# Kernel tuning notes

Hardware: AMD Instinct MI355X
Metric: run time of the kernel (lower is better)

The kernel has to match this reference:

```python
import jax, jax.numpy as jnp
import numpy as np

B, H, W = 8, 1080, 1920


def setup_inputs() -> dict:
    key = jax.random.key(0)
    k1, k2 = jax.random.split(key)
    flow = jax.random.normal(k1, (B, 2, H, W), jnp.float32) * 10.0  # ~10px motion
    depth = jax.random.uniform(k2, (B, 1, H, W), jnp.float32) + 0.1  # positive weight
    return {"flow": flow, "depth": depth}


def _splat_avg(flow, depth):
    """Depth-weighted forward splat of -flow to the 4 integer pixels around the
    projected location (x+fx, y+fy), accumulate a weight buffer, then average."""
    Bn, _, Hn, Wn = flow.shape
    fx, fy = flow[:, 0], flow[:, 1]                 # [B,H,W]
    col = jnp.arange(Wn, dtype=flow.dtype)
    row = jnp.arange(Hn, dtype=flow.dtype)[:, None]
    x2 = col + fx
    y2 = row + fy
    valid = (x2 >= 0) & (x2 <= Wn - 1) & (y2 >= 0) & (y2 <= Hn - 1)
    ixL = jnp.clip(jnp.floor(x2).astype(jnp.int32), 0, Wn - 1)
    iyT = jnp.clip(jnp.floor(y2).astype(jnp.int32), 0, Hn - 1)
    ixR = jnp.minimum(ixL + 1, Wn - 1)
    iyB = jnp.minimum(iyT + 1, Hn - 1)
    w = jnp.where(valid, depth[:, 0], 0.0)          # depth weight, 0 if off-frame
    b_off = (jnp.arange(Bn, dtype=jnp.int32) * (Hn * Wn))[:, None, None]
    corners = [(iyT, ixL), (iyT, ixR), (iyB, ixL), (iyB, ixR)]
    lin = jnp.stack([b_off + iy * Wn + ix for iy, ix in corners]).reshape(-1)  # [4*B*H*W]
    vals = jnp.stack([-fx * w, -fy * w, w])         # [3,B,H,W]
    vals = jnp.broadcast_to(vals[:, None], (3, 4, Bn, Hn, Wn)).reshape(3, -1)
    acc = jnp.zeros((3, Bn * Hn * Wn), flow.dtype).at[:, lin].add(vals)
    out = acc[:2].reshape(2, Bn, Hn, Wn).transpose(1, 0, 2, 3)   # [B,2,H,W]
    count = acc[2].reshape(Bn, 1, Hn, Wn)                        # [B,1,H,W]
    denom = jnp.where(count > 0, count, 1.0)
    out = out / denom                                            # avg pass
    return out, count


def _fillhole(out, count):
    """For hole pixels (count==0), average the nearest filled pixel found in
    each of the 4 axis directions (left/right/up/down), equal weights."""
    mask = count[:, 0] > 0                           # [B,H,W]
    Bn, Hn, Wn = mask.shape
    col = jnp.arange(Wn, dtype=jnp.int32)
    row = jnp.arange(Hn, dtype=jnp.int32)[:, None]

    a = jnp.where(mask, col, -1)
    incl = jax.lax.associative_scan(jnp.maximum, a, axis=2)
    left = jnp.pad(incl[:, :, :-1], ((0, 0), (0, 0), (1, 0)), constant_values=-1)
    a = jnp.where(mask, col, Wn)
    incl = jax.lax.associative_scan(jnp.minimum, a, axis=2, reverse=True)
    right = jnp.pad(incl[:, :, 1:], ((0, 0), (0, 0), (0, 1)), constant_values=Wn)
    a = jnp.where(mask, row, -1)
    incl = jax.lax.associative_scan(jnp.maximum, a, axis=1)
    up = jnp.pad(incl[:, :-1, :], ((0, 0), (1, 0), (0, 0)), constant_values=-1)
    a = jnp.where(mask, row, Hn)
    incl = jax.lax.associative_scan(jnp.minimum, a, axis=1, reverse=True)
    down = jnp.pad(incl[:, 1:, :], ((0, 0), (0, 1), (0, 0)), constant_values=Hn)

    def gather(idx, axis, bound):
        found = ((idx >= 0) & (idx < bound))[:, None]        # [B,1,H,W]
        ic = jnp.clip(idx, 0, bound - 1)[:, None]
        v = jnp.take_along_axis(out, jnp.broadcast_to(ic, out.shape), axis=axis)
        return v, found.astype(out.dtype)

    vl, wl = gather(left, 3, Wn)
    vr, wr = gather(right, 3, Wn)
    vu, wu = gather(up, 2, Hn)
    vd, wd = gather(down, 2, Hn)
    s = wl + wr + wu + wd
    fill = (wl * vl + wr * vr + wu * vu + wd * vd) / jnp.maximum(s, 1.0)
    hole = (~mask)[:, None]
    return jnp.where(hole & (s > 0), fill, out)


def reference(flow, depth):
    out, count = _splat_avg(flow, depth)
    out = _fillhole(out, count)   # torch module runs fillhole when requires_grad=False
    return out
```

## Files before the change

### kernel.cpp

```cpp
#include <hip/hip_runtime.h>

#define BB 8
#define HH 1080
#define WW 1920
constexpr int HWc  = HH * WW;
constexpr int Ntot = BB * HWc;

constexpr int TILE = 64;
constexpr int MAR  = 32;
constexpr int REG  = TILE + 2 * MAR;
constexpr int WT   = WW / TILE;
constexpr int HT   = (HH + TILE - 1) / TILE;
constexpr int NTILE = WT * HT;
constexpr int GT    = NTILE * BB;
constexpr int CAP   = 256;

constexpr int SDIM = 65;
constexpr int SSTR = 66;
constexpr int PL   = SSTR * SSTR;

static_assert(TILE == 64, "ownership test uses >>6");
static_assert((WW & 3) == 0 && (HWc & 3) == 0, "float4 groups must not straddle");
static_assert(3 * PL * 4 <= 53000, "need 3 blocks/CU");

constexpr size_t OFF_BKT  = 16384;
constexpr size_t OFF_MASK = OFF_BKT + (size_t)GT * CAP * 16;
constexpr size_t OFF_W    = OFF_MASK + (size_t)Ntot;
static_assert(OFF_W % 16 == 0, "wplane must be float4-aligned");

__device__ inline void spill_append(int b, int xs, int ys, int ixL, int iyT,
                                    float fx, float fy, float w,
                                    unsigned* cnt, float4* buckets) {
    int ixR = min(ixL + 1, WW - 1);
    int iyB = min(iyT + 1, HH - 1);
    int cxs[2] = {ixL, ixR};
    int cys[2] = {iyT, iyB};
    float vx = -fx * w, vy = -fy * w;
#pragma unroll
    for (int a = 0; a < 2; ++a)
#pragma unroll
        for (int cc = 0; cc < 2; ++cc) {
            int cx = cxs[cc], cy = cys[a];
            int ox = (cx >> 6) * TILE - MAR;
            int oy = (cy >> 6) * TILE - MAR;
            if (!(xs >= ox && xs < ox + REG && ys >= oy && ys < oy + REG)) {
                int gtile = b * NTILE + (cy >> 6) * WT + (cx >> 6);
                unsigned slot = atomicAdd(&cnt[gtile], 1u);
                if (slot < (unsigned)CAP) {
                    float4 rec;
                    rec.x = __int_as_float(((cy & 63) << 6) | (cx & 63));
                    rec.y = vx; rec.z = vy; rec.w = w;
                    buckets[(size_t)gtile * CAP + slot] = rec;
                }
            }
        }
}

#define PROC(FXC, FYC, DWC, CGX)                                               \
    {                                                                          \
        float fx = (FXC), fy = (FYC);                                          \
        float x2 = (float)(CGX) + fx, y2 = gyf + fy;                           \
        if (x2 >= 0.f && x2 <= (float)(WW - 1) &&                              \
            y2 >= 0.f && y2 <= (float)(HH - 1)) {                              \
            int ixL = (int)floorf(x2);        \
            int iyT = (int)floorf(y2);                                         \
            unsigned cI = (unsigned)(ixL - (X0 - 1));                          \
            unsigned rI = (unsigned)(iyT - (Y0 - 1));                          \
            if (cI < (unsigned)SDIM && rI < (unsigned)SDIM) {                  \
                float w = (DWC);                                               \
                if (ixL == WW - 1) w += w;      \
                if (iyT == HH - 1) w += w;      \
                int cell = (int)(rI * SSTR + cI);                              \
                atomicAdd(&sm[cell],          -fx * w);                        \
                atomicAdd(&sm[cell + PL],     -fy * w);                        \
                atomicAdd(&sm[cell + 2 * PL], w);                              \
            }                                                                  \
            if (core && (fabsf(fx) > 30.f || fabsf(fy) > 30.f))                \
                spill_append(b, (CGX), gy, ixL, iyT, fx, fy, (DWC),            \
                             cnt, buckets);                                    \
        }                                                                      \
    }

__global__ __launch_bounds__(512, 6) void tile_k(const float* __restrict__ flow,
                                                 const float* __restrict__ depth,
                                                 unsigned* __restrict__ cnt,
                                                 float4* __restrict__ buckets,
                                                 float* __restrict__ out,
                                                 unsigned char* __restrict__ mask,
                                                 float* __restrict__ wplane) {
    __shared__ float sm[3 * PL];
    const int bid  = blockIdx.x;
    const int b    = bid & 7;
    const int tile = bid >> 3;
    const int ty   = tile / WT;
    const int tx   = tile - ty * WT;
    const int X0 = tx * TILE, Y0 = ty * TILE;
    const int rx0 = X0 - MAR, ry0 = Y0 - MAR;
    const int tid = threadIdx.x;

    float4* sm4 = (float4*)sm;
    for (int i = tid; i < 3 * PL / 4; i += 512)
        sm4[i] = make_float4(0.f, 0.f, 0.f, 0.f);
    __syncthreads();

    const float* fxp = flow + (size_t)b * 2 * HWc;
    const float* fyp = fxp + HWc;
    const float* dp  = depth + (size_t)b * HWc;

    const int gx  = rx0 + ((tid & 31) << 2);
    const bool xok = (unsigned)gx < (unsigned)WW;
    const bool xin = (unsigned)(gx - X0) < (unsigned)TILE;
    int gy = ry0 + (tid >> 5);
    float4 cfx, cfy, cd;
    bool ok = xok && ((unsigned)gy < (unsigned)HH);
    if (ok) {
        int p = gy * WW + gx;
        cfx = *(const float4*)(fxp + p);
        cfy = *(const float4*)(fyp + p);
        cd  = *(const float4*)(dp + p);
    }
#pragma unroll
    for (int k = 0; k < 8; ++k) {
        float4 nfx, nfy, nd;
        bool nok = false;
        const int ngy = gy + 16;
        if (k < 7) {
            nok = xok && ((unsigned)ngy < (unsigned)HH);
            if (nok) {
                int np = ngy * WW + gx;
                nfx = *(const float4*)(fxp + np);
                nfy = *(const float4*)(fyp + np);
                nd  = *(const float4*)(dp + np);
            }
        }
        if (ok) {
            const float gyf = (float)gy;
            const bool core = xin && ((unsigned)(gy - Y0) < (unsigned)TILE);
            PROC(cfx.x, cfy.x, cd.x, gx)
            PROC(cfx.y, cfy.y, cd.y, gx + 1)
            PROC(cfx.z, cfy.z, cd.z, gx + 2)
            PROC(cfx.w, cfy.w, cd.w, gx + 3)
        }
        ok = nok; gy = ngy; cfx = nfx; cfy = nfy; cd = nd;
    }
    __syncthreads();

    float* o0 = out + (size_t)b * 2 * HWc;
    float* o1 = o0 + HWc;
    float* wp = wplane + (size_t)b * HWc;
    unsigned char* mb = mask + (size_t)b * HWc;
#pragma unroll
    for (int k = 0; k < 2; ++k) {
        int j   = k * 512 + tid;
        int row = j >> 4;
        int gy2 = Y0 + row;
        if (gy2 < HH) {
            int c0 = (j & 15) << 2;
            int q  = gy2 * WW + X0 + c0;
            const int rA = (row + 1) * SSTR + c0;
            const int rB = row * SSTR + c0;
            float4 vx, vy, wv;
            {
                float a_0 = sm[rA], a_1 = sm[rA+1], a_2 = sm[rA+2], a_3 = sm[rA+3], a_4 = sm[rA+4];
                float b_0 = sm[rB], b_1 = sm[rB+1], b_2 = sm[rB+2], b_3 = sm[rB+3], b_4 = sm[rB+4];
                vx.x = a_0+a_1+b_0+b_1; vx.y = a_1+a_2+b_1+b_2;
                vx.z = a_2+a_3+b_2+b_3; vx.w = a_3+a_4+b_3+b_4;
            }
            {
                const int oA = rA + PL, oB = rB + PL;
                float a_0 = sm[oA], a_1 = sm[oA+1], a_2 = sm[oA+2], a_3 = sm[oA+3], a_4 = sm[oA+4];
                float b_0 = sm[oB], b_1 = sm[oB+1], b_2 = sm[oB+2], b_3 = sm[oB+3], b_4 = sm[oB+4];
                vy.x = a_0+a_1+b_0+b_1; vy.y = a_1+a_2+b_1+b_2;
                vy.z = a_2+a_3+b_2+b_3; vy.w = a_3+a_4+b_3+b_4;
            }
            {
                const int oA = rA + 2 * PL, oB = rB + 2 * PL;
                float a_0 = sm[oA], a_1 = sm[oA+1], a_2 = sm[oA+2], a_3 = sm[oA+3], a_4 = sm[oA+4];
                float b_0 = sm[oB], b_1 = sm[oB+1], b_2 = sm[oB+2], b_3 = sm[oB+3], b_4 = sm[oB+4];
                wv.x = a_0+a_1+b_0+b_1; wv.y = a_1+a_2+b_1+b_2;
                wv.z = a_2+a_3+b_2+b_3; wv.w = a_3+a_4+b_3+b_4;
            }
            float i0 = wv.x > 0.f ? 1.f / wv.x : 0.f;
            float i1 = wv.y > 0.f ? 1.f / wv.y : 0.f;
            float i2 = wv.z > 0.f ? 1.f / wv.z : 0.f;
            float i3 = wv.w > 0.f ? 1.f / wv.w : 0.f;
            float4 r0, r1;
            r0.x = vx.x * i0; r0.y = vx.y * i1; r0.z = vx.z * i2; r0.w = vx.w * i3;
            r1.x = vy.x * i0; r1.y = vy.y * i1; r1.z = vy.z * i2; r1.w = vy.w * i3;
            *(float4*)(o0 + q) = r0;
            *(float4*)(o1 + q) = r1;
            *(float4*)(wp + q) = wv;
            uchar4 mk;
            mk.x = (unsigned char)(wv.x > 0.f);
            mk.y = (unsigned char)(wv.y > 0.f);
            mk.z = (unsigned char)(wv.z > 0.f);
            mk.w = (unsigned char)(wv.w > 0.f);
            *(uchar4*)(mb + q) = mk;
        }
    }
}

__global__ __launch_bounds__(256) void fixup_k(const unsigned* __restrict__ cnt,
                                               const float4* __restrict__ buckets,
                                               float* __restrict__ out,
                                               const float* __restrict__ wplane,
                                               unsigned char* __restrict__ mask) {
    __shared__ float s[3 * 4096];
    int gtile = blockIdx.x;
    unsigned n = cnt[gtile];
    if (n == 0) return;
    if (n > (unsigned)CAP) n = CAP;
    int b  = gtile / NTILE;
    int t  = gtile - b * NTILE;
    int ty = t / WT, tx = t - ty * WT;
    int X0 = tx * TILE, Y0 = ty * TILE;

    float4* s4 = (float4*)s;
    for (int i = threadIdx.x; i < 3 * 4096 / 4; i += 256)
        s4[i] = make_float4(0.f, 0.f, 0.f, 0.f);
    __syncthreads();

    const float4* bkt = buckets + (size_t)gtile * CAP;
    for (unsigned r = threadIdx.x; r < n; r += 256) {
        float4 rec = bkt[r];
        int cell = __float_as_int(rec.x);
        atomicAdd(&s[cell],        rec.y);
        atomicAdd(&s[cell + 4096], rec.z);
        atomicAdd(&s[cell + 8192], rec.w);
    }
    __syncthreads();

    float* o0 = out + (size_t)b * 2 * HWc;
    float* o1 = o0 + HWc;
    const float* wp = wplane + (size_t)b * HWc;
    unsigned char* mb = mask + (size_t)b * HWc;
    for (int cell = threadIdx.x; cell < 4096; cell += 256) {
        float ws = s[cell + 8192];
        if (ws != 0.f) {
            int cy = Y0 + (cell >> 6), cx = X0 + (cell & 63);
            if (cy < HH) {
                int q = cy * WW + cx;
                float w0 = wp[q];
                float wn = w0 + ws;
                float v0 = o0[q] * w0 + s[cell];
                float v1 = o1[q] * w0 + s[cell + 4096];
                float inv = wn > 0.f ? 1.f / wn : 0.f;
                o0[q] = v0 * inv;
                o1[q] = v1 * inv;
                mb[q] = 1;
            }
        }
    }
}

__global__ __launch_bounds__(256) void fill_k(float* __restrict__ out,
                                              const unsigned char* __restrict__ mask) {
    constexpr int NG = Ntot / 4;
    int g = blockIdx.x * 256 + threadIdx.x;
    if (g >= NG) return;
    int idx0 = g << 2;
    uchar4 m4 = *(const uchar4*)(mask + idx0);
    if (m4.x & m4.y & m4.z & m4.w) return;

    int b = idx0 / HWc;
    int p0 = idx0 - b * HWc;
    int y = p0 / WW;
    int x0 = p0 - y * WW;

    const unsigned char* mb = mask + (size_t)b * HWc;
    const float* o0 = out + (size_t)b * 2 * HWc;
    const float* o1 = o0 + HWc;
    const unsigned char ms[4] = {m4.x, m4.y, m4.z, m4.w};

#pragma unroll
    for (int c = 0; c < 4; ++c) {
        if (ms[c]) continue;
        int x = x0 + c;
        int p = p0 + c;
        float s = 0.f, s0 = 0.f, s1 = 0.f;
        for (int j = x - 1; j >= 0; --j) {
            if (mb[y * WW + j]) { int q = y * WW + j; s += 1.f; s0 += o0[q]; s1 += o1[q]; break; }
        }
        for (int j = x + 1; j < WW; ++j) {
            if (mb[y * WW + j]) { int q = y * WW + j; s += 1.f; s0 += o0[q]; s1 += o1[q]; break; }
        }
        for (int i = y - 1; i >= 0; --i) {
            if (mb[i * WW + x]) { int q = i * WW + x; s += 1.f; s0 += o0[q]; s1 += o1[q]; break; }
        }
        for (int i = y + 1; i < HH; ++i) {
            if (mb[i * WW + x]) { int q = i * WW + x; s += 1.f; s0 += o0[q]; s1 += o1[q]; break; }
        }
        if (s > 0.f) {
            ((float*)o0)[p] = s0 / s;
            ((float*)o1)[p] = s1 / s;
        }
    }
}

extern "C" void kernel_launch(void* const* d_in, const int* in_sizes, int n_in,
                              void* d_out, int out_size, void* d_ws, size_t ws_size,
                              hipStream_t stream) {
    const float* flow  = (const float*)d_in[0];
    const float* depth = (const float*)d_in[1];
    float* out = (float*)d_out;

    unsigned char* wsb = (unsigned char*)d_ws;
    unsigned* cnt       = (unsigned*)wsb;
    float4*  buckets    = (float4*)(wsb + OFF_BKT);
    unsigned char* mask = wsb + OFF_MASK;
    float*   wplane     = (float*)(wsb + OFF_W);

    const int threads = 256;

    hipMemsetAsync(cnt, 0, (size_t)GT * sizeof(unsigned), stream);

    tile_k<<<GT, 512, 0, stream>>>(flow, depth, cnt, buckets, out, mask, wplane);

    fixup_k<<<GT, threads, 0, stream>>>(cnt, buckets, out, wplane, mask);

    fill_k<<<(Ntot / 4 + threads - 1) / threads, threads, 0, stream>>>(out, mask);
}
```

Measured before the change: 606.9 us.

## Stage tile mask window in LDS for hole-fill neighbor search

The hole-fill kernel now runs one block per 64x64 output tile and batch image. Each block first copies a 128x128 mask window (the tile plus a 32-pixel margin) into shared memory. The four directional nearest-filled-pixel searches scan that shared window first and fall back to global memory only when the search leaves it. This removes repeated strided byte reads from global memory, especially in the vertical scans. In exchange, each block pays a staging cost and a barrier, and threads diverge when hole pixels are sparse within a tile.

```diff
diff --git a/kernel.cpp b/kernel.cpp
--- a/kernel.cpp
+++ b/kernel.cpp
@@ -253,44 +253,97 @@
     }
 }
 
+constexpr int FWW = 128;
 __global__ __launch_bounds__(256) void fill_k(float* __restrict__ out,
                                               const unsigned char* __restrict__ mask) {
-    constexpr int NG = Ntot / 4;
-    int g = blockIdx.x * 256 + threadIdx.x;
-    if (g >= NG) return;
-    int idx0 = g << 2;
-    uchar4 m4 = *(const uchar4*)(mask + idx0);
-    if (m4.x & m4.y & m4.z & m4.w) return;
-
-    int b = idx0 / HWc;
-    int p0 = idx0 - b * HWc;
-    int y = p0 / WW;
-    int x0 = p0 - y * WW;
+    __shared__ unsigned char wm[FWW * FWW];
+    const int bid  = blockIdx.x;
+    const int b    = bid & 7;
+    const int tile = bid >> 3;
+    const int ty   = tile / WT;
+    const int tx   = tile - ty * WT;
+    const int X0 = tx * TILE, Y0 = ty * TILE;
+    const int wx0 = X0 - 32, wy0 = Y0 - 32;
+    const int tid = threadIdx.x;
 
     const unsigned char* mb = mask + (size_t)b * HWc;
+
+    {
+        int r  = tid >> 1, h = tid & 1;
+        int wy = wy0 + r;
+        int xs = wx0 + h * 64;
+        unsigned char* dst = &wm[r * FWW + h * 64];
+        if ((unsigned)wy >= (unsigned)HH) {
+            uint4 z = make_uint4(0u, 0u, 0u, 0u);
+            uint4* d4 = (uint4*)dst;
+            d4[0] = z; d4[1] = z; d4[2] = z; d4[3] = z;
+        } else if (xs >= 0 && xs + 64 <= WW) {
+            const uint4* s4 = (const uint4*)(mb + (size_t)wy * WW + xs);
+            uint4* d4 = (uint4*)dst;
+            d4[0] = s4[0]; d4[1] = s4[1]; d4[2] = s4[2]; d4[3] = s4[3];
+        } else {
+            for (int i = 0; i < 64; ++i) {
+                int gxx = xs + i;
+                dst[i] = ((unsigned)gxx < (unsigned)WW)
+                             ? mb[(size_t)wy * WW + gxx] : (unsigned char)0;
+            }
+        }
+    }
+    __syncthreads();
+
     const float* o0 = out + (size_t)b * 2 * HWc;
     const float* o1 = o0 + HWc;
-    const unsigned char ms[4] = {m4.x, m4.y, m4.z, m4.w};
-
-#pragma unroll
-    for (int c = 0; c < 4; ++c) {
-        if (ms[c]) continue;
-        int x = x0 + c;
-        int p = p0 + c;
+
+    for (int k = 0; k < 16; ++k) {
+        int ci = k * 256 + tid;
+        int ry = ci >> 6, cx = ci & 63;
+        int gy = Y0 + ry;
+        if (gy >= HH) continue;
+        int wr = ry + 32, wc = cx + 32;
+        if (wm[wr * FWW + wc]) continue;
+
+        int gxp = X0 + cx;
         float s = 0.f, s0 = 0.f, s1 = 0.f;
-        for (int j = x - 1; j >= 0; --j) {
-            if (mb[y * WW + j]) { int q = y * WW + j; s += 1.f; s0 += o0[q]; s1 += o1[q]; break; }
-        }
-        for (int j = x + 1; j < WW; ++j) {
-            if (mb[y * WW + j]) { int q = y * WW + j; s += 1.f; s0 += o0[q]; s1 += o1[q]; break; }
-        }
-        for (int i = y - 1; i >= 0; --i) {
-            if (mb[i * WW + x]) { int q = i * WW + x; s += 1.f; s0 += o0[q]; s1 += o1[q]; break; }
-        }
-        for (int i = y + 1; i < HH; ++i) {
-            if (mb[i * WW + x]) { int q = i * WW + x; s += 1.f; s0 += o0[q]; s1 += o1[q]; break; }
-        }
+
+        {
+            int f = -1;
+            for (int j = wc - 1; j >= 0; --j)
+                if (wm[wr * FWW + j]) { f = wx0 + j; break; }
+            if (f < 0 && wx0 > 0)
+                for (int j = wx0 - 1; j >= 0; --j)
+                    if (mb[(size_t)gy * WW + j]) { f = j; break; }
+            if (f >= 0) { int q = gy * WW + f; s += 1.f; s0 += o0[q]; s1 += o1[q]; }
+        }
+        {
+            int f = -1;
+            for (int j = wc + 1; j < FWW; ++j)
+                if (wm[wr * FWW + j]) { f = wx0 + j; break; }
+            if (f < 0 && wx0 + FWW < WW)
+                for (int j = wx0 + FWW; j < WW; ++j)
+                    if (mb[(size_t)gy * WW + j]) { f = j; break; }
+            if (f >= 0) { int q = gy * WW + f; s += 1.f; s0 += o0[q]; s1 += o1[q]; }
+        }
+        {
+            int f = -1;
+            for (int i = wr - 1; i >= 0; --i)
+                if (wm[i * FWW + wc]) { f = wy0 + i; break; }
+            if (f < 0 && wy0 > 0)
+                for (int i = wy0 - 1; i >= 0; --i)
+                    if (mb[(size_t)i * WW + gxp]) { f = i; break; }
+            if (f >= 0) { int q = f * WW + gxp; s += 1.f; s0 += o0[q]; s1 += o1[q]; }
+        }
+        {
+            int f = -1;
+            for (int i = wr + 1; i < FWW; ++i)
+                if (wm[i * FWW + wc]) { f = wy0 + i; break; }
+            if (f < 0 && wy0 + FWW < HH)
+                for (int i = wy0 + FWW; i < HH; ++i)
+                    if (mb[(size_t)i * WW + gxp]) { f = i; break; }
+            if (f >= 0) { int q = f * WW + gxp; s += 1.f; s0 += o0[q]; s1 += o1[q]; }
+        }
+
         if (s > 0.f) {
+            int p = gy * WW + gxp;
             ((float*)o0)[p] = s0 / s;
             ((float*)o1)[p] = s1 / s;
         }
@@ -318,5 +371,5 @@
 
     fixup_k<<<GT, threads, 0, stream>>>(cnt, buckets, out, wplane, mask);
 
-    fill_k<<<(Ntot / 4 + threads - 1) / threads, threads, 0, stream>>>(out, mask);
-}
+    fill_k<<<GT, threads, 0, stream>>>(out, mask);
+}
```

Result: no change. 597.3 us (-1.6%).
